# Optimization experiments

Hardware: AMD Instinct MI355X
Metric: run time of the kernel (lower is better)

## Reference

```python
import jax, jax.numpy as jnp
import numpy as np

B, L, G, P, K = 16, 2048, 8, 8, 64
CLAMP = 15.0


def _cdist(x, y):
    # Euclidean pairwise distance: x [..., K, 3], y [..., L, 3] -> [..., K, L]
    x2 = jnp.sum(x * x, axis=-1)[..., :, None]
    y2 = jnp.sum(y * y, axis=-1)[..., None, :]
    xy = jnp.einsum('...kc,...lc->...kl', x, y)
    return jnp.sqrt(jnp.maximum(x2 + y2 - 2.0 * xy, 0.0))


def setup_inputs() -> dict:
    key = jax.random.key(0)
    k1, k2, k3 = jax.random.split(key, 3)
    rng = np.random.default_rng(0)
    # each group: K distinct atom indices; each of the P rows is a permutation of them
    auto = np.empty((G, P, K), dtype=np.int64)
    for g in range(G):
        base = rng.permutation(L)[:K]
        auto[g, 0] = base
        for j in range(1, P):
            auto[g, j] = base[rng.permutation(K)]
    return {
        'x_pred': jax.random.normal(k1, (B, L, 3), jnp.float32),
        'x_native': jax.random.normal(k2, (B, L, 3), jnp.float32),
        'x_native_mask': jax.random.randint(k3, (B, L), 0, 2).astype(bool),
        'automorphs': jnp.asarray(auto),
    }


def reference(x_pred, x_native, x_native_mask, automorphs):
    Bn, Ln = x_pred.shape[0], x_pred.shape[1]
    Kn = automorphs.shape[-1]
    batch_idx = jnp.arange(Bn)
    denom = jnp.asarray(Kn * (Ln - Kn), x_pred.dtype)

    def step(carry, a):
        x_nat, nat_mask = carry
        a0 = a[0]                                           # [K]
        # columns NOT in the symmetry group (the ~mask columns)
        colmask = jnp.ones((Ln,), x_pred.dtype).at[a0].set(0.0)
        d_pred = _cdist(x_pred[:, a0], x_pred)              # [B,K,L]
        gath = x_nat[:, a]                                  # [B,P,K,3]
        d_nat = _cdist(gath, x_nat[:, None])                # [B,P,K,L]
        drms = jnp.minimum(jnp.nan_to_num(jnp.square(d_pred[:, None] - d_nat)), CLAMP)
        drms = jnp.sum(drms * colmask, axis=(-1, -2)) / denom   # [B,P] masked mean
        bestj = jnp.argmin(drms, axis=1)                    # first min <=> strict-< update
        sel = gath[batch_idx, bestj]                        # [B,K,3]
        sel_m = nat_mask[:, a][batch_idx, bestj]            # [B,K]
        x_nat = x_nat.at[:, a0].set(sel)
        nat_mask = nat_mask.at[:, a0].set(sel_m)
        return (x_nat, nat_mask), None

    (x_nat, nat_mask), _ = jax.lax.scan(step, (x_native, x_native_mask), automorphs)
    return x_nat, nat_mask
```

## Files before the change

### kernel.cpp

```cpp
#include <hip/hip_runtime.h>
#include <math.h>

#define Bn 16
#define Ln 2048
#define Gn 8
#define Pn 8
#define Kn 64
#define CLAMP_V 15.0f

#define BPB 32
#define NTH 512
#define NWV (NTH / 64)
#define LPB (Ln / BPB)
#define LPW (LPB / NWV)
#define PK  (Pn * Kn)

#define MAGIC(g) (0x5EED0000u | (unsigned)(g))

typedef unsigned long long ull;

__device__ __forceinline__ float wave_sum64(float x) {
#define DPP_ADD(ctrl) \
    x += __int_as_float(__builtin_amdgcn_update_dpp(0, __float_as_int(x), ctrl, 0xf, 0xf, true))
    DPP_ADD(0x111);
    DPP_ADD(0x112);
    DPP_ADD(0x114);
    DPP_ADD(0x118);
    DPP_ADD(0x142);
    DPP_ADD(0x143);
#undef DPP_ADD
    return x;
}

template <int IMM>
__device__ __forceinline__ float swz_xor(float v) {
    return v + __int_as_float(__builtin_amdgcn_ds_swizzle(__float_as_int(v), IMM));
}
__device__ __forceinline__ ull ld_rlx64(const ull* p) {
    return __hip_atomic_load(p, __ATOMIC_RELAXED, __HIP_MEMORY_SCOPE_AGENT);
}
__device__ __forceinline__ void st_rlx64(ull* p, ull v) {
    __hip_atomic_store(p, v, __ATOMIC_RELAXED, __HIP_MEMORY_SCOPE_AGENT);
}

__global__ __launch_bounds__(NTH, 2) void fused_kernel(
    const float* __restrict__ xpred, const float* __restrict__ xnat,
    const int* __restrict__ mask_in, const int* __restrict__ autom,
    float* __restrict__ out_x, float* __restrict__ out_m,
    ull* __restrict__ part) {

    const int tid  = threadIdx.x;
    const int lane = tid & 63;
    const int wv   = tid >> 6;
    const int bid  = blockIdx.x;
    const int b    = (bid & 7) | ((bid >> 8) << 3);
    const int c    = (bid >> 3) & 31;

    __shared__ float4         s_all[Ln];
    __shared__ unsigned short s_idx[Ln];
    __shared__ unsigned char  s_inv[2][Ln];
    __shared__ float4         s_xp[LPB];
    __shared__ float          s_part[NWV][Pn];
    __shared__ float2         s_dn2[NWV][Kn];

    const float* xpb = xpred + (size_t)b * Ln * 3;
    const float* xnb = xnat  + (size_t)b * Ln * 3;

    for (int l = tid; l < Ln; l += NTH) {
        s_idx[l] = (unsigned short)l;
        s_all[l] = make_float4(xnb[l * 3 + 0], xnb[l * 3 + 1], xnb[l * 3 + 2], 0.0f);
    }
    if (wv == 0) {
        const int l = c * LPB + lane;
        s_xp[lane] = make_float4(xpb[l * 3 + 0], xpb[l * 3 + 1], xpb[l * 3 + 2], 0.0f);
    } else if (wv == 2) {
        s_inv[0][autom[lane]] = (unsigned char)lane;
    }
    int   a0k = autom[lane];
    float px = xpb[a0k * 3 + 0], py = xpb[a0k * 3 + 1], pz = xpb[a0k * 3 + 2];
    __syncthreads();

    #pragma unroll 1
    for (int g = 0; g < Gn; g++) {
        const int* ag  = autom + g * PK;
        const int* ag1 = autom + (g + 1) * PK;
        const int  cur = g & 1, nxt = cur ^ 1;
        ull* pg = part + (size_t)(g * Bn + b) * (BPB * Pn);

        const float4 nk = s_all[s_idx[a0k]];
        const float2 cxp = make_float2(px, nk.x);
        const float2 cyp = make_float2(py, nk.y);
        const float2 czp = make_float2(pz, nk.z);
        float2* const dnrow = s_dn2[wv];
        int sid[Pn];
        #pragma unroll
        for (int p = 0; p < Pn; p++)
            sid[p] = (int)s_inv[cur][ag[p * Kn + lane]];
        unsigned short jl[LPW];
        #pragma unroll
        for (int i = 0; i < LPW; i++)
            jl[i] = s_idx[c * LPB + wv * LPW + i];

        float acc[Pn];
        #pragma unroll
        for (int p = 0; p < Pn; p++) acc[p] = 0.0f;

        #pragma unroll
        for (int ii = 0; ii < LPW; ii += 2) {
            const int il0 = wv * LPW + ii;
            const int l0  = c * LPB + il0;
            const bool sk0 = __ballot(a0k == l0)     != 0ull;
            const bool sk1 = __ballot(a0k == l0 + 1) != 0ull;
            if (sk0 && sk1) continue;

            const float4 q0 = s_xp[il0],      q1 = s_xp[il0 + 1];
            const float4 m0 = s_all[jl[ii]],  m1 = s_all[jl[ii + 1]];
            const float2 ux0 = cxp - make_float2(q0.x, m0.x);
            const float2 uy0 = cyp - make_float2(q0.y, m0.y);
            const float2 uz0 = czp - make_float2(q0.z, m0.z);
            const float2 ss0 = ux0 * ux0 + uy0 * uy0 + uz0 * uz0;
            const float2 ux1 = cxp - make_float2(q1.x, m1.x);
            const float2 uy1 = cyp - make_float2(q1.y, m1.y);
            const float2 uz1 = czp - make_float2(q1.z, m1.z);
            const float2 ss1 = ux1 * ux1 + uy1 * uy1 + uz1 * uz1;
            const float dp0 = __builtin_amdgcn_sqrtf(ss0.x);
            const float dn0 = __builtin_amdgcn_sqrtf(ss0.y);
            const float dp1 = __builtin_amdgcn_sqrtf(ss1.x);
            const float dn1 = __builtin_amdgcn_sqrtf(ss1.y);
            dnrow[lane] = make_float2(dn0, dn1);
            const float2 dpp    = make_float2(dp0, dp1);
            const float2 dn_own = make_float2(dn0, dn1);

            if (!(sk0 | sk1)) {
                {
                    const float2 e = dpp - dn_own;
                    const float2 s = e * e;
                    acc[0] += fminf(s.x, CLAMP_V);
                    acc[0] += fminf(s.y, CLAMP_V);
                }
                #pragma unroll
                for (int p = 1; p < Pn; p++) {
                    const float2 dns = dnrow[sid[p]];
                    const float2 e = dpp - dns;
                    const float2 s = e * e;
                    acc[p] += fminf(s.x, CLAMP_V);
                    acc[p] += fminf(s.y, CLAMP_V);
                }
            } else {
                const float w0 = sk0 ? 0.0f : 1.0f;
                const float w1 = sk1 ? 0.0f : 1.0f;
                {
                    const float2 e = dpp - dn_own;
                    const float2 s = e * e;
                    acc[0] += fminf(s.x, CLAMP_V) * w0;
                    acc[0] += fminf(s.y, CLAMP_V) * w1;
                }
                #pragma unroll
                for (int p = 1; p < Pn; p++) {
                    const float2 dns = dnrow[sid[p]];
                    const float2 e = dpp - dns;
                    const float2 s = e * e;
                    acc[p] += fminf(s.x, CLAMP_V) * w0;
                    acc[p] += fminf(s.y, CLAMP_V) * w1;
                }
            }
        }

        #pragma unroll
        for (int p = 0; p < Pn; p++) {
            const float v = wave_sum64(acc[p]);
            if (lane == 63) s_part[wv][p] = v;
        }
        __syncthreads();

        if (wv == 0) {
            float v = s_part[lane >> 3][lane & 7];
            v = swz_xor<0x201F>(v);
            v = swz_xor<0x401F>(v);
            v += __shfl(v, lane + 32, 64);
            if (lane < 8)
                st_rlx64(&pg[c * Pn + lane],
                         ((ull)MAGIC(g) << 32) | (ull)__float_as_uint(v));
        }

        if (g < Gn - 1) {
            a0k = ag1[lane];
            px = xpb[a0k * 3 + 0]; py = xpb[a0k * 3 + 1]; pz = xpb[a0k * 3 + 2];
            if (wv == 2) s_inv[nxt][ag1[lane]] = (unsigned char)lane;
        }

        if (wv == 0) {
            const unsigned magic = MAGIC(g);
            ull q0 = 0, q1 = 0, q2 = 0, q3 = 0;
            bool r0 = false, r1 = false, r2 = false, r3 = false;
            for (;;) {
                if (!r0) { q0 = ld_rlx64(pg + lane);       r0 = (unsigned)(q0 >> 32) == magic; }
                if (!r1) { q1 = ld_rlx64(pg + lane + 64);  r1 = (unsigned)(q1 >> 32) == magic; }
                if (!r2) { q2 = ld_rlx64(pg + lane + 128); r2 = (unsigned)(q2 >> 32) == magic; }
                if (!r3) { q3 = ld_rlx64(pg + lane + 192); r3 = (unsigned)(q3 >> 32) == magic; }
                if (__ballot(!(r0 && r1 && r2 && r3)) == 0ull) break;
                __builtin_amdgcn_s_sleep(1);
            }
            float v = __uint_as_float((unsigned)q0) + __uint_as_float((unsigned)q1)
                    + __uint_as_float((unsigned)q2) + __uint_as_float((unsigned)q3);
            v = swz_xor<0x201F>(v);
            v = swz_xor<0x401F>(v);
            v += __shfl(v, lane + 32, 64);
            float best = __shfl(v, 0, 64);
            int   bj   = 0;
            #pragma unroll
            for (int p = 1; p < Pn; p++) {
                const float t = __shfl(v, p, 64);
                if (t < best) { best = t; bj = p; }
            }
            const unsigned short oldv = s_idx[ag[bj * Kn + lane]];
            s_idx[ag[lane]] = oldv;
        }
        __syncthreads();
    }

    const int l0 = c * LPB;
    if (tid < LPB * 3) {
        const int ll = tid / 3, coord = tid % 3;
        const int l  = l0 + ll;
        const float4 v = s_all[s_idx[l]];
        out_x[((size_t)b * Ln + l) * 3 + coord] =
            (coord == 0) ? v.x : ((coord == 1) ? v.y : v.z);
    } else if (tid < LPB * 4) {
        const int l = l0 + (tid - LPB * 3);
        const int j = s_idx[l];
        out_m[(size_t)b * Ln + l] = (float)mask_in[(size_t)b * Ln + j];
    }
}

extern "C" void kernel_launch(void* const* d_in, const int* in_sizes, int n_in,
                              void* d_out, int out_size, void* d_ws, size_t ws_size,
                              hipStream_t stream) {
    const float* xpred   = (const float*)d_in[0];
    const float* xnat_in = (const float*)d_in[1];
    const int*   mask_in = (const int*)  d_in[2];
    const int*   autom   = (const int*)  d_in[3];

    float* out_x = (float*)d_out;
    float* out_m = out_x + Bn * Ln * 3;

    ull* part = (ull*)d_ws;

    fused_kernel<<<Bn * BPB, NTH, 0, stream>>>(
        xpred, xnat_in, mask_in, autom, out_x, out_m, part);
}
```

Measured before the change: 100.7 us.

## Publish per-wave partials globally and process four columns per iteration

```diff
diff --git a/kernel.cpp b/kernel.cpp
--- a/kernel.cpp
+++ b/kernel.cpp
@@ -60,8 +60,7 @@
     __shared__ unsigned short s_idx[Ln];
     __shared__ unsigned char  s_inv[2][Ln];
     __shared__ float4         s_xp[LPB];
-    __shared__ float          s_part[NWV][Pn];
-    __shared__ float2         s_dn2[NWV][Kn];
+    __shared__ float4         s_dn4[NWV][Kn];
 
     const float* xpb = xpred + (size_t)b * Ln * 3;
     const float* xnb = xnat  + (size_t)b * Ln * 3;
@@ -85,13 +84,13 @@
         const int* ag  = autom + g * PK;
         const int* ag1 = autom + (g + 1) * PK;
         const int  cur = g & 1, nxt = cur ^ 1;
-        ull* pg = part + (size_t)(g * Bn + b) * (BPB * Pn);
+        ull* pg = part + (size_t)(g * Bn + b) * (BPB * NWV * Pn);
 
         const float4 nk = s_all[s_idx[a0k]];
         const float2 cxp = make_float2(px, nk.x);
         const float2 cyp = make_float2(py, nk.y);
         const float2 czp = make_float2(pz, nk.z);
-        float2* const dnrow = s_dn2[wv];
+        float4* const dnrow = s_dn4[wv];
         int sid[Pn];
         #pragma unroll
         for (int p = 0; p < Pn; p++)
@@ -106,15 +105,19 @@
         for (int p = 0; p < Pn; p++) acc[p] = 0.0f;
 
         #pragma unroll
-        for (int ii = 0; ii < LPW; ii += 2) {
+        for (int ii = 0; ii < LPW; ii += 4) {
             const int il0 = wv * LPW + ii;
             const int l0  = c * LPB + il0;
             const bool sk0 = __ballot(a0k == l0)     != 0ull;
             const bool sk1 = __ballot(a0k == l0 + 1) != 0ull;
-            if (sk0 && sk1) continue;
-
-            const float4 q0 = s_xp[il0],      q1 = s_xp[il0 + 1];
-            const float4 m0 = s_all[jl[ii]],  m1 = s_all[jl[ii + 1]];
+            const bool sk2 = __ballot(a0k == l0 + 2) != 0ull;
+            const bool sk3 = __ballot(a0k == l0 + 3) != 0ull;
+            if (sk0 && sk1 && sk2 && sk3) continue;
+
+            const float4 q0 = s_xp[il0],          q1 = s_xp[il0 + 1];
+            const float4 q2 = s_xp[il0 + 2],      q3 = s_xp[il0 + 3];
+            const float4 m0 = s_all[jl[ii]],      m1 = s_all[jl[ii + 1]];
+            const float4 m2 = s_all[jl[ii + 2]],  m3 = s_all[jl[ii + 3]];
             const float2 ux0 = cxp - make_float2(q0.x, m0.x);
             const float2 uy0 = cyp - make_float2(q0.y, m0.y);
             const float2 uz0 = czp - make_float2(q0.z, m0.z);
@@ -123,64 +126,77 @@
             const float2 uy1 = cyp - make_float2(q1.y, m1.y);
             const float2 uz1 = czp - make_float2(q1.z, m1.z);
             const float2 ss1 = ux1 * ux1 + uy1 * uy1 + uz1 * uz1;
+            const float2 ux2 = cxp - make_float2(q2.x, m2.x);
+            const float2 uy2 = cyp - make_float2(q2.y, m2.y);
+            const float2 uz2 = czp - make_float2(q2.z, m2.z);
+            const float2 ss2 = ux2 * ux2 + uy2 * uy2 + uz2 * uz2;
+            const float2 ux3 = cxp - make_float2(q3.x, m3.x);
+            const float2 uy3 = cyp - make_float2(q3.y, m3.y);
+            const float2 uz3 = czp - make_float2(q3.z, m3.z);
+            const float2 ss3 = ux3 * ux3 + uy3 * uy3 + uz3 * uz3;
             const float dp0 = __builtin_amdgcn_sqrtf(ss0.x);
             const float dn0 = __builtin_amdgcn_sqrtf(ss0.y);
             const float dp1 = __builtin_amdgcn_sqrtf(ss1.x);
             const float dn1 = __builtin_amdgcn_sqrtf(ss1.y);
-            dnrow[lane] = make_float2(dn0, dn1);
-            const float2 dpp    = make_float2(dp0, dp1);
-            const float2 dn_own = make_float2(dn0, dn1);
-
-            if (!(sk0 | sk1)) {
+            const float dp2 = __builtin_amdgcn_sqrtf(ss2.x);
+            const float dn2 = __builtin_amdgcn_sqrtf(ss2.y);
+            const float dp3 = __builtin_amdgcn_sqrtf(ss3.x);
+            const float dn3 = __builtin_amdgcn_sqrtf(ss3.y);
+            dnrow[lane] = make_float4(dn0, dn1, dn2, dn3);
+
+            if (!(sk0 | sk1 | sk2 | sk3)) {
                 {
-                    const float2 e = dpp - dn_own;
-                    const float2 s = e * e;
-                    acc[0] += fminf(s.x, CLAMP_V);
-                    acc[0] += fminf(s.y, CLAMP_V);
+                    const float e0 = dp0 - dn0, e1 = dp1 - dn1;
+                    const float e2 = dp2 - dn2, e3 = dp3 - dn3;
+                    acc[0] += fminf(e0 * e0, CLAMP_V);
+                    acc[0] += fminf(e1 * e1, CLAMP_V);
+                    acc[0] += fminf(e2 * e2, CLAMP_V);
+                    acc[0] += fminf(e3 * e3, CLAMP_V);
                 }
                 #pragma unroll
                 for (int p = 1; p < Pn; p++) {
-                    const float2 dns = dnrow[sid[p]];
-                    const float2 e = dpp - dns;
-                    const float2 s = e * e;
-                    acc[p] += fminf(s.x, CLAMP_V);
-                    acc[p] += fminf(s.y, CLAMP_V);
+                    const float4 dns = dnrow[sid[p]];
+                    const float e0 = dp0 - dns.x, e1 = dp1 - dns.y;
+                    const float e2 = dp2 - dns.z, e3 = dp3 - dns.w;
+                    acc[p] += fminf(e0 * e0, CLAMP_V);
+                    acc[p] += fminf(e1 * e1, CLAMP_V);
+                    acc[p] += fminf(e2 * e2, CLAMP_V);
+                    acc[p] += fminf(e3 * e3, CLAMP_V);
                 }
             } else {
                 const float w0 = sk0 ? 0.0f : 1.0f;
                 const float w1 = sk1 ? 0.0f : 1.0f;
+                const float w2 = sk2 ? 0.0f : 1.0f;
+                const float w3 = sk3 ? 0.0f : 1.0f;
                 {
-                    const float2 e = dpp - dn_own;
-                    const float2 s = e * e;
-                    acc[0] += fminf(s.x, CLAMP_V) * w0;
-                    acc[0] += fminf(s.y, CLAMP_V) * w1;
+                    const float e0 = dp0 - dn0, e1 = dp1 - dn1;
+                    const float e2 = dp2 - dn2, e3 = dp3 - dn3;
+                    acc[0] += fminf(e0 * e0, CLAMP_V) * w0;
+                    acc[0] += fminf(e1 * e1, CLAMP_V) * w1;
+                    acc[0] += fminf(e2 * e2, CLAMP_V) * w2;
+                    acc[0] += fminf(e3 * e3, CLAMP_V) * w3;
                 }
                 #pragma unroll
                 for (int p = 1; p < Pn; p++) {
-                    const float2 dns = dnrow[sid[p]];
-                    const float2 e = dpp - dns;
-                    const float2 s = e * e;
-                    acc[p] += fminf(s.x, CLAMP_V) * w0;
-                    acc[p] += fminf(s.y, CLAMP_V) * w1;
-                }
-            }
-        }
-
-        #pragma unroll
-        for (int p = 0; p < Pn; p++) {
-            const float v = wave_sum64(acc[p]);
-            if (lane == 63) s_part[wv][p] = v;
-        }
-        __syncthreads();
-
-        if (wv == 0) {
-            float v = s_part[lane >> 3][lane & 7];
-            v = swz_xor<0x201F>(v);
-            v = swz_xor<0x401F>(v);
-            v += __shfl(v, lane + 32, 64);
-            if (lane < 8)
-                st_rlx64(&pg[c * Pn + lane],
-                         ((ull)MAGIC(g) << 32) | (ull)__float_as_uint(v));
+                    const float4 dns = dnrow[sid[p]];
+                    const float e0 = dp0 - dns.x, e1 = dp1 - dns.y;
+                    const float e2 = dp2 - dns.z, e3 = dp3 - dns.w;
+                    acc[p] += fminf(e0 * e0, CLAMP_V) * w0;
+                    acc[p] += fminf(e1 * e1, CLAMP_V) * w1;
+                    acc[p] += fminf(e2 * e2, CLAMP_V) * w2;
+                    acc[p] += fminf(e3 * e3, CLAMP_V) * w3;
+                }
+            }
+        }
+
+        float vv[Pn];
+        #pragma unroll
+        for (int p = 0; p < Pn; p++) vv[p] = wave_sum64(acc[p]);
+        if (lane == 63) {
+            ull* dst = pg + ((size_t)(c * NWV + wv)) * Pn;
+            #pragma unroll
+            for (int p = 0; p < Pn; p++)
+                st_rlx64(&dst[p], ((ull)MAGIC(g) << 32) | (ull)__float_as_uint(vv[p]));
         }
 
         if (g < Gn - 1) {
@@ -191,18 +207,34 @@
 
         if (wv == 0) {
             const unsigned magic = MAGIC(g);
-            ull q0 = 0, q1 = 0, q2 = 0, q3 = 0;
-            bool r0 = false, r1 = false, r2 = false, r3 = false;
+            ull qa[16];
             for (;;) {
-                if (!r0) { q0 = ld_rlx64(pg + lane);       r0 = (unsigned)(q0 >> 32) == magic; }
-                if (!r1) { q1 = ld_rlx64(pg + lane + 64);  r1 = (unsigned)(q1 >> 32) == magic; }
-                if (!r2) { q2 = ld_rlx64(pg + lane + 128); r2 = (unsigned)(q2 >> 32) == magic; }
-                if (!r3) { q3 = ld_rlx64(pg + lane + 192); r3 = (unsigned)(q3 >> 32) == magic; }
-                if (__ballot(!(r0 && r1 && r2 && r3)) == 0ull) break;
+                bool all = true;
+                #pragma unroll
+                for (int m = 0; m < 16; m++) {
+                    qa[m] = ld_rlx64(pg + lane + 64 * m);
+                    all &= ((unsigned)(qa[m] >> 32) == magic);
+                }
+                if (__ballot(!all) == 0ull) break;
                 __builtin_amdgcn_s_sleep(1);
             }
-            float v = __uint_as_float((unsigned)q0) + __uint_as_float((unsigned)q1)
-                    + __uint_as_float((unsigned)q2) + __uint_as_float((unsigned)q3);
+            float s0 = 0.0f;
+            #pragma unroll
+            for (int m = 0; m < 16; m++) s0 += __uint_as_float((unsigned)qa[m]);
+            for (;;) {
+                bool all = true;
+                #pragma unroll
+                for (int m = 0; m < 16; m++) {
+                    qa[m] = ld_rlx64(pg + lane + 64 * (16 + m));
+                    all &= ((unsigned)(qa[m] >> 32) == magic);
+                }
+                if (__ballot(!all) == 0ull) break;
+                __builtin_amdgcn_s_sleep(1);
+            }
+            float s1 = 0.0f;
+            #pragma unroll
+            for (int m = 0; m < 16; m++) s1 += __uint_as_float((unsigned)qa[m]);
+            float v = s0 + s1;
             v = swz_xor<0x201F>(v);
             v = swz_xor<0x401F>(v);
             v += __shfl(v, lane + 32, 64);
```

Result: slower. 174.8 us (+73.5%).

## Add dedicated coordinator wave for cross-block reduction and argmin

Applied to the files above, without the earlier changes.

```diff
diff --git a/kernel.cpp b/kernel.cpp
--- a/kernel.cpp
+++ b/kernel.cpp
@@ -9,10 +9,10 @@
 #define CLAMP_V 15.0f
 
 #define BPB 32
-#define NTH 512
-#define NWV (NTH / 64)
+#define NTH 576
+#define NCW 8
 #define LPB (Ln / BPB)
-#define LPW (LPB / NWV)
+#define LPW (LPB / NCW)
 #define PK  (Pn * Kn)
 
 #define MAGIC(g) (0x5EED0000u | (unsigned)(g))
@@ -36,6 +36,10 @@
 __device__ __forceinline__ float swz_xor(float v) {
     return v + __int_as_float(__builtin_amdgcn_ds_swizzle(__float_as_int(v), IMM));
 }
+template <int IMM>
+__device__ __forceinline__ float swz_min(float v) {
+    return fminf(v, __int_as_float(__builtin_amdgcn_ds_swizzle(__float_as_int(v), IMM)));
+}
 __device__ __forceinline__ ull ld_rlx64(const ull* p) {
     return __hip_atomic_load(p, __ATOMIC_RELAXED, __HIP_MEMORY_SCOPE_AGENT);
 }
@@ -60,12 +64,14 @@
     __shared__ unsigned short s_idx[Ln];
     __shared__ unsigned char  s_inv[2][Ln];
     __shared__ float4         s_xp[LPB];
-    __shared__ float          s_part[NWV][Pn];
-    __shared__ float2         s_dn2[NWV][Kn];
+    __shared__ float          s_part[NCW][Pn];
+    __shared__ float2         s_dn2[NCW][Kn];
+    __shared__ int            s_cnt;
 
     const float* xpb = xpred + (size_t)b * Ln * 3;
     const float* xnb = xnat  + (size_t)b * Ln * 3;
 
+    if (tid == 0) s_cnt = 0;
     for (int l = tid; l < Ln; l += NTH) {
         s_idx[l] = (unsigned short)l;
         s_all[l] = make_float4(xnb[l * 3 + 0], xnb[l * 3 + 1], xnb[l * 3 + 2], 0.0f);
@@ -87,132 +93,163 @@
         const int  cur = g & 1, nxt = cur ^ 1;
         ull* pg = part + (size_t)(g * Bn + b) * (BPB * Pn);
 
-        const float4 nk = s_all[s_idx[a0k]];
-        const float2 cxp = make_float2(px, nk.x);
-        const float2 cyp = make_float2(py, nk.y);
-        const float2 czp = make_float2(pz, nk.z);
-        float2* const dnrow = s_dn2[wv];
-        int sid[Pn];
-        #pragma unroll
-        for (int p = 0; p < Pn; p++)
-            sid[p] = (int)s_inv[cur][ag[p * Kn + lane]];
-        unsigned short jl[LPW];
-        #pragma unroll
-        for (int i = 0; i < LPW; i++)
-            jl[i] = s_idx[c * LPB + wv * LPW + i];
-
-        float acc[Pn];
-        #pragma unroll
-        for (int p = 0; p < Pn; p++) acc[p] = 0.0f;
-
-        #pragma unroll
-        for (int ii = 0; ii < LPW; ii += 2) {
-            const int il0 = wv * LPW + ii;
-            const int l0  = c * LPB + il0;
-            const bool sk0 = __ballot(a0k == l0)     != 0ull;
-            const bool sk1 = __ballot(a0k == l0 + 1) != 0ull;
-            if (sk0 && sk1) continue;
-
-            const float4 q0 = s_xp[il0],      q1 = s_xp[il0 + 1];
-            const float4 m0 = s_all[jl[ii]],  m1 = s_all[jl[ii + 1]];
-            const float2 ux0 = cxp - make_float2(q0.x, m0.x);
-            const float2 uy0 = cyp - make_float2(q0.y, m0.y);
-            const float2 uz0 = czp - make_float2(q0.z, m0.z);
-            const float2 ss0 = ux0 * ux0 + uy0 * uy0 + uz0 * uz0;
-            const float2 ux1 = cxp - make_float2(q1.x, m1.x);
-            const float2 uy1 = cyp - make_float2(q1.y, m1.y);
-            const float2 uz1 = czp - make_float2(q1.z, m1.z);
-            const float2 ss1 = ux1 * ux1 + uy1 * uy1 + uz1 * uz1;
-            const float dp0 = __builtin_amdgcn_sqrtf(ss0.x);
-            const float dn0 = __builtin_amdgcn_sqrtf(ss0.y);
-            const float dp1 = __builtin_amdgcn_sqrtf(ss1.x);
-            const float dn1 = __builtin_amdgcn_sqrtf(ss1.y);
-            dnrow[lane] = make_float2(dn0, dn1);
-            const float2 dpp    = make_float2(dp0, dp1);
-            const float2 dn_own = make_float2(dn0, dn1);
-
-            if (!(sk0 | sk1)) {
-                {
-                    const float2 e = dpp - dn_own;
-                    const float2 s = e * e;
-                    acc[0] += fminf(s.x, CLAMP_V);
-                    acc[0] += fminf(s.y, CLAMP_V);
+        if (wv < NCW) {
+            const float4 nk = s_all[s_idx[a0k]];
+            const float2 cxp = make_float2(px, nk.x);
+            const float2 cyp = make_float2(py, nk.y);
+            const float2 czp = make_float2(pz, nk.z);
+            float2* const dnrow = s_dn2[wv];
+            int sid[Pn];
+            #pragma unroll
+            for (int p = 0; p < Pn; p++)
+                sid[p] = (int)s_inv[cur][ag[p * Kn + lane]];
+            unsigned short jl[LPW];
+            #pragma unroll
+            for (int i = 0; i < LPW; i++)
+                jl[i] = s_idx[c * LPB + wv * LPW + i];
+
+            float acc[Pn];
+            #pragma unroll
+            for (int p = 0; p < Pn; p++) acc[p] = 0.0f;
+
+            #pragma unroll
+            for (int ii = 0; ii < LPW; ii += 2) {
+                const int il0 = wv * LPW + ii;
+                const int l0  = c * LPB + il0;
+                const bool sk0 = __ballot(a0k == l0)     != 0ull;
+                const bool sk1 = __ballot(a0k == l0 + 1) != 0ull;
+                if (sk0 && sk1) continue;
+
+                const float4 q0 = s_xp[il0],      q1 = s_xp[il0 + 1];
+                const float4 m0 = s_all[jl[ii]],  m1 = s_all[jl[ii + 1]];
+                const float2 ux0 = cxp - make_float2(q0.x, m0.x);
+                const float2 uy0 = cyp - make_float2(q0.y, m0.y);
+                const float2 uz0 = czp - make_float2(q0.z, m0.z);
+                const float2 ss0 = ux0 * ux0 + uy0 * uy0 + uz0 * uz0;
+                const float2 ux1 = cxp - make_float2(q1.x, m1.x);
+                const float2 uy1 = cyp - make_float2(q1.y, m1.y);
+                const float2 uz1 = czp - make_float2(q1.z, m1.z);
+                const float2 ss1 = ux1 * ux1 + uy1 * uy1 + uz1 * uz1;
+                const float dp0 = __builtin_amdgcn_sqrtf(ss0.x);
+                const float dn0 = __builtin_amdgcn_sqrtf(ss0.y);
+                const float dp1 = __builtin_amdgcn_sqrtf(ss1.x);
+                const float dn1 = __builtin_amdgcn_sqrtf(ss1.y);
+                dnrow[lane] = make_float2(dn0, dn1);
+                const float2 dpp    = make_float2(dp0, dp1);
+                const float2 dn_own = make_float2(dn0, dn1);
+
+                if (!(sk0 | sk1)) {
+                    {
+                        const float2 e = dpp - dn_own;
+                        const float2 s = e * e;
+                        acc[0] += fminf(s.x, CLAMP_V);
+                        acc[0] += fminf(s.y, CLAMP_V);
+                    }
+                    #pragma unroll
+                    for (int p = 1; p < Pn; p++) {
+                        const float2 dns = dnrow[sid[p]];
+                        const float2 e = dpp - dns;
+                        const float2 s = e * e;
+                        acc[p] += fminf(s.x, CLAMP_V);
+                        acc[p] += fminf(s.y, CLAMP_V);
+                    }
+                } else {
+                    const float w0 = sk0 ? 0.0f : 1.0f;
+                    const float w1 = sk1 ? 0.0f : 1.0f;
+                    {
+                        const float2 e = dpp - dn_own;
+                        const float2 s = e * e;
+                        acc[0] += fminf(s.x, CLAMP_V) * w0;
+                        acc[0] += fminf(s.y, CLAMP_V) * w1;
+                    }
+                    #pragma unroll
+                    for (int p = 1; p < Pn; p++) {
+                        const float2 dns = dnrow[sid[p]];
+                        const float2 e = dpp - dns;
+                        const float2 s = e * e;
+                        acc[p] += fminf(s.x, CLAMP_V) * w0;
+                        acc[p] += fminf(s.y, CLAMP_V) * w1;
+                    }
                 }
+            }
+
+            #pragma unroll
+            for (int p = 0; p < Pn; p++) {
+                const float v = wave_sum64(acc[p]);
+                if (lane == 63) s_part[wv][p] = v;
+            }
+            if (lane == 63) atomicAdd(&s_cnt, 1);
+
+            if (g < Gn - 1) {
+                a0k = ag1[lane];
+                px = xpb[a0k * 3 + 0]; py = xpb[a0k * 3 + 1]; pz = xpb[a0k * 3 + 2];
+                if (wv == 2) s_inv[nxt][ag1[lane]] = (unsigned char)lane;
+            }
+        } else {
+            const unsigned magic = MAGIC(g);
+            const int target = NCW * (g + 1);
+            ull  qv[4];
+            bool rdy[4];
+            int  ownm = -1;
+            #pragma unroll
+            for (int m = 0; m < 4; m++) {
+                const int idx = lane + 64 * m;
+                const bool own = ((idx >> 3) == c);
+                rdy[m] = own;
+                if (own) ownm = m;
+                qv[m] = 0;
+            }
+            for (;;) {
+                bool all = true;
                 #pragma unroll
-                for (int p = 1; p < Pn; p++) {
-                    const float2 dns = dnrow[sid[p]];
-                    const float2 e = dpp - dns;
-                    const float2 s = e * e;
-                    acc[p] += fminf(s.x, CLAMP_V);
-                    acc[p] += fminf(s.y, CLAMP_V);
+                for (int m = 0; m < 4; m++) {
+                    if (!rdy[m]) {
+                        qv[m] = ld_rlx64(pg + lane + 64 * m);
+                        rdy[m] = ((unsigned)(qv[m] >> 32) == magic);
+                        all &= rdy[m];
+                    }
                 }
-            } else {
-                const float w0 = sk0 ? 0.0f : 1.0f;
-                const float w1 = sk1 ? 0.0f : 1.0f;
-                {
-                    const float2 e = dpp - dn_own;
-                    const float2 s = e * e;
-                    acc[0] += fminf(s.x, CLAMP_V) * w0;
-                    acc[0] += fminf(s.y, CLAMP_V) * w1;
-                }
-                #pragma unroll
-                for (int p = 1; p < Pn; p++) {
-                    const float2 dns = dnrow[sid[p]];
-                    const float2 e = dpp - dns;
-                    const float2 s = e * e;
-                    acc[p] += fminf(s.x, CLAMP_V) * w0;
-                    acc[p] += fminf(s.y, CLAMP_V) * w1;
-                }
-            }
-        }
-
-        #pragma unroll
-        for (int p = 0; p < Pn; p++) {
-            const float v = wave_sum64(acc[p]);
-            if (lane == 63) s_part[wv][p] = v;
-        }
-        __syncthreads();
-
-        if (wv == 0) {
-            float v = s_part[lane >> 3][lane & 7];
-            v = swz_xor<0x201F>(v);
-            v = swz_xor<0x401F>(v);
-            v += __shfl(v, lane + 32, 64);
+                if (__ballot(!all) == 0ull) break;
+                if (__hip_atomic_load(&s_cnt, __ATOMIC_RELAXED,
+                                      __HIP_MEMORY_SCOPE_WORKGROUP) >= target) break;
+                __builtin_amdgcn_s_sleep(4);
+            }
+            while (__hip_atomic_load(&s_cnt, __ATOMIC_RELAXED,
+                                     __HIP_MEMORY_SCOPE_WORKGROUP) < target)
+                __builtin_amdgcn_s_sleep(0);
+            float vf = s_part[lane >> 3][lane & 7];
+            vf = swz_xor<0x201F>(vf);
+            vf = swz_xor<0x401F>(vf);
+            vf += __shfl(vf, lane + 32, 64);
             if (lane < 8)
                 st_rlx64(&pg[c * Pn + lane],
-                         ((ull)MAGIC(g) << 32) | (ull)__float_as_uint(v));
-        }
-
-        if (g < Gn - 1) {
-            a0k = ag1[lane];
-            px = xpb[a0k * 3 + 0]; py = xpb[a0k * 3 + 1]; pz = xpb[a0k * 3 + 2];
-            if (wv == 2) s_inv[nxt][ag1[lane]] = (unsigned char)lane;
-        }
-
-        if (wv == 0) {
-            const unsigned magic = MAGIC(g);
-            ull q0 = 0, q1 = 0, q2 = 0, q3 = 0;
-            bool r0 = false, r1 = false, r2 = false, r3 = false;
+                         ((ull)MAGIC(g) << 32) | (ull)__float_as_uint(vf));
             for (;;) {
-                if (!r0) { q0 = ld_rlx64(pg + lane);       r0 = (unsigned)(q0 >> 32) == magic; }
-                if (!r1) { q1 = ld_rlx64(pg + lane + 64);  r1 = (unsigned)(q1 >> 32) == magic; }
-                if (!r2) { q2 = ld_rlx64(pg + lane + 128); r2 = (unsigned)(q2 >> 32) == magic; }
-                if (!r3) { q3 = ld_rlx64(pg + lane + 192); r3 = (unsigned)(q3 >> 32) == magic; }
-                if (__ballot(!(r0 && r1 && r2 && r3)) == 0ull) break;
+                bool all = true;
+                #pragma unroll
+                for (int m = 0; m < 4; m++) {
+                    if (!rdy[m]) {
+                        qv[m] = ld_rlx64(pg + lane + 64 * m);
+                        rdy[m] = ((unsigned)(qv[m] >> 32) == magic);
+                        all &= rdy[m];
+                    }
+                }
+                if (__ballot(!all) == 0ull) break;
                 __builtin_amdgcn_s_sleep(1);
             }
-            float v = __uint_as_float((unsigned)q0) + __uint_as_float((unsigned)q1)
-                    + __uint_as_float((unsigned)q2) + __uint_as_float((unsigned)q3);
-            v = swz_xor<0x201F>(v);
-            v = swz_xor<0x401F>(v);
-            v += __shfl(v, lane + 32, 64);
-            float best = __shfl(v, 0, 64);
-            int   bj   = 0;
-            #pragma unroll
-            for (int p = 1; p < Pn; p++) {
-                const float t = __shfl(v, p, 64);
-                if (t < best) { best = t; bj = p; }
-            }
+            const float vown = __shfl(vf, lane & 7, 64);
+            float s = 0.0f;
+            #pragma unroll
+            for (int m = 0; m < 4; m++)
+                s += (m == ownm) ? vown : __uint_as_float((unsigned)qv[m]);
+            s = swz_xor<0x201F>(s);
+            s = swz_xor<0x401F>(s);
+            s += __shfl(s, lane + 32, 64);
+            float mn = swz_min<0x041F>(s);
+            mn = swz_min<0x081F>(mn);
+            mn = swz_min<0x101F>(mn);
+            const ull mk = __ballot(s == mn) & 0xFFull;
+            const int bj = (int)__builtin_ctzll(mk);
             const unsigned short oldv = s_idx[ag[bj * Kn + lane]];
             s_idx[ag[lane]] = oldv;
         }
```

After: 133.1 us. 32.1% more time.
